# Kernel tuning notes

Hardware: AMD Instinct MI355X
Metric: run time of the kernel (lower is better)

## Reference

```python
import jax, jax.numpy as jnp
import numpy as np

B, N, H = 2, 4096, 1024
HEADS, DHEAD, M = 16, 64, 256
KERNEL_EPS = 1e-3


def setup_inputs() -> dict:
    key = jax.random.key(0)
    ks = jax.random.split(key, 10)
    w = lambda k, shp: jax.random.normal(k, shp, dtype=jnp.float32) * 0.02
    return {
        "hidden_states": jax.random.normal(ks[0], (B, N, H), dtype=jnp.float32),
        "Wq": w(ks[1], (H, H)), "bq": jnp.zeros((H,), jnp.float32),
        "Wk": w(ks[2], (H, H)), "bk": jnp.zeros((H,), jnp.float32),
        "Wv": w(ks[3], (H, H)), "bv": jnp.zeros((H,), jnp.float32),
        "Wo": w(ks[4], (H, H)), "bo": jnp.zeros((H,), jnp.float32),
        "proj": jax.random.normal(ks[5], (M, DHEAD), dtype=jnp.float32),
    }


def _split_heads(x):
    b, n, _ = x.shape
    return x.reshape(b, n, HEADS, DHEAD).transpose(0, 2, 1, 3)  # [b,h,n,d]


def _softmax_kernel(data, proj, is_query):
    # data: [b,h,n,d]; proj: [m,d]
    data_normalizer = DHEAD ** (-0.25)
    data_dash = jnp.einsum('bhnd,md->bhnm', data_normalizer * data, proj)
    diag_data = -0.5 * jnp.sum(data * data, axis=-1, keepdims=True)  # [b,h,n,1]
    if is_query:
        # argmax over a size-1 last dim -> stabilizer == diag_data itself
        stab = diag_data
    else:
        stab = jnp.max(diag_data)
    kernel_out = jnp.exp(diag_data + (data_dash - stab))  # exp kernel: exp(h + x)
    return (M ** (-0.5)) * (kernel_out + KERNEL_EPS)


def _performer_forward(hidden_states, Wq, bq, Wk, bk, Wv, bv, Wo, bo, proj):
    q = _split_heads(jnp.einsum('bni,oi->bno', hidden_states, Wq) + bq)
    k = _split_heads(jnp.einsum('bni,oi->bno', hidden_states, Wk) + bk)
    v = _split_heads(jnp.einsum('bni,oi->bno', hidden_states, Wv) + bv)

    qf = _softmax_kernel(q, proj, is_query=True)   # [b,h,n,m]
    kf = _softmax_kernel(k, proj, is_query=False)  # [b,h,n,m]

    # linear_attention (non-causal FAVOR+)
    k_cumsum = kf.sum(axis=-2)                                   # [b,h,m]
    d_inv = 1.0 / jnp.einsum('bhnm,bhm->bhn', qf, k_cumsum)      # [b,h,n]
    context = jnp.einsum('bhnm,bhne->bhme', kf, v)               # [b,h,m,d]
    out = jnp.einsum('bhme,bhnm,bhn->bhne', context, qf, d_inv)  # [b,h,n,d]

    out = out.transpose(0, 2, 1, 3).reshape(hidden_states.shape[0], -1, H)
    return jnp.einsum('bni,oi->bno', out, Wo) + bo


def reference(hidden_states, Wq, bq, Wk, bk, Wv, bv, Wo, bo, proj):
    return _performer_forward(hidden_states, Wq, bq, Wk, bk, Wv, bv, Wo, bo, proj)
```

## Files before the change

kernel.cpp:

```cpp
#include <hip/hip_runtime.h>
#include <math.h>

#define B_      2
#define N_      4096
#define H_      1024
#define HEADS_  16
#define DH_     64
#define M_      256
#define NSPLIT  8
#define EPAD    80

constexpr float NORMALIZER = 0.35355339059327373f;
constexpr float RATIO      = 0.0625f;
constexpr float KEPS       = 1e-3f;

typedef __bf16 bf16x8 __attribute__((ext_vector_type(8)));
typedef __bf16 bf16x4 __attribute__((ext_vector_type(4)));
typedef float  f32x4  __attribute__((ext_vector_type(4)));

__global__ __launch_bounds__(256) void split_bf16(
    const float* __restrict__ src, __bf16* __restrict__ hi, __bf16* __restrict__ lo)
{
    int i = blockIdx.x * 256 + threadIdx.x;
    float4 v = ((const float4*)src)[i];
    float vv[4] = {v.x, v.y, v.z, v.w};
    bf16x4 h, l;
#pragma unroll
    for (int j = 0; j < 4; ++j) {
        __bf16 hh = (__bf16)vv[j];
        h[j] = hh;
        l[j] = (__bf16)(vv[j] - (float)hh);
    }
    ((bf16x4*)hi)[i] = h;
    ((bf16x4*)lo)[i] = l;
}

__global__ __launch_bounds__(256) void split_w(
    const float* __restrict__ W0, const float* __restrict__ W1,
    const float* __restrict__ W2, const float* __restrict__ W3,
    __bf16* __restrict__ hi, __bf16* __restrict__ lo)
{
    const float* src = W0;
    if (blockIdx.y == 1) src = W1;
    else if (blockIdx.y == 2) src = W2;
    else if (blockIdx.y == 3) src = W3;
    int i = blockIdx.x * 256 + threadIdx.x;
    size_t o = (size_t)blockIdx.y * 262144 + i;
    float4 v = ((const float4*)src)[i];
    float vv[4] = {v.x, v.y, v.z, v.w};
    bf16x4 h, l;
#pragma unroll
    for (int j = 0; j < 4; ++j) {
        __bf16 hh = (__bf16)vv[j];
        h[j] = hh;
        l[j] = (__bf16)(vv[j] - (float)hh);
    }
    ((bf16x4*)hi)[o] = h;
    ((bf16x4*)lo)[o] = l;
}

__global__ __launch_bounds__(512, 2) void gemm_qkv(
    const __bf16* __restrict__ Ah, const __bf16* __restrict__ Al,
    const __bf16* __restrict__ WH, const __bf16* __restrict__ WL,
    const float* __restrict__ bq, const float* __restrict__ bk, const float* __restrict__ bv,
    __bf16* __restrict__ Qh, __bf16* __restrict__ Ql,
    __bf16* __restrict__ Kh, __bf16* __restrict__ Kl,
    __bf16* __restrict__ Vh, __bf16* __restrict__ Vl)
{
    __shared__ alignas(16) __bf16 lds[2][8][128 * 32];

    const int t    = threadIdx.x;
    const int lane = t & 63;
    const int lm   = lane & 15;
    const int lq   = lane >> 4;
    const int w    = t >> 6;
    const int wm   = (w >> 2) * 64;
    const int wn   = (w & 3) * 32;

    const int wg = blockIdx.x + 8 * blockIdx.y;
    const int sw = (wg & 7) * 64 + (wg >> 3);
    const int n0 = (sw & 7) * 128;
    const int m0 = (sw >> 3) * 128;
    const int K  = 1024;
    const int NK = 32;
    const size_t WSZ = (size_t)H_ * H_;

    const __bf16* mysrc;
    if      (w == 0) mysrc = Ah;
    else if (w == 1) mysrc = Al;
    else             mysrc = ((w & 1) ? WL : WH) + (size_t)((w - 2) >> 1) * WSZ;
    const int rbase  = (w < 2) ? m0 : n0;
    const int rsub   = lane >> 2;
    const int slot   = lane & 3;
    const int schunk = slot ^ ((lane >> 3) & 3);
    const __bf16* gbase = mysrc + (size_t)(rbase + rsub) * K + schunk * 8;

    f32x4 acc[3][4][2];
#pragma unroll
    for (int s = 0; s < 3; ++s)
#pragma unroll
        for (int i = 0; i < 4; ++i)
#pragma unroll
            for (int j = 0; j < 2; ++j) acc[s][i][j] = (f32x4){0.f, 0.f, 0.f, 0.f};

    const int swz = (lq ^ ((lm >> 1) & 3)) * 8;

    auto stage = [&](int buf, int k0) {
#pragma unroll
        for (int c = 0; c < 8; ++c) {
            const __bf16* g = gbase + (size_t)c * 16 * K + k0;
            __builtin_amdgcn_global_load_lds(
                (const __attribute__((address_space(1))) void*)g,
                (__attribute__((address_space(3))) void*)&lds[buf][w][c * 512],
                16, 0, 0);
        }
    };

    auto compute = [&](int p) {
        bf16x8 bh[3][2], bl[3][2];
#pragma unroll
        for (int s = 0; s < 3; ++s)
#pragma unroll
            for (int j = 0; j < 2; ++j) {
                int off = (wn + j * 16 + lm) * 32 + swz;
                bh[s][j] = *(const bf16x8*)&lds[p][2 + 2 * s][off];
                bl[s][j] = *(const bf16x8*)&lds[p][3 + 2 * s][off];
            }
#pragma unroll
        for (int i = 0; i < 4; ++i) {
            int off = (wm + i * 16 + lm) * 32 + swz;
            bf16x8 ah = *(const bf16x8*)&lds[p][0][off];
            bf16x8 al = *(const bf16x8*)&lds[p][1][off];
#pragma unroll
            for (int s = 0; s < 3; ++s)
#pragma unroll
                for (int j = 0; j < 2; ++j) {
                    acc[s][i][j] = __builtin_amdgcn_mfma_f32_16x16x32_bf16(ah, bh[s][j], acc[s][i][j], 0, 0, 0);
                    acc[s][i][j] = __builtin_amdgcn_mfma_f32_16x16x32_bf16(al, bh[s][j], acc[s][i][j], 0, 0, 0);
                    acc[s][i][j] = __builtin_amdgcn_mfma_f32_16x16x32_bf16(ah, bl[s][j], acc[s][i][j], 0, 0, 0);
                }
        }
    };

    stage(0, 0);
    int p = 0;
#pragma unroll 1
    for (int kk = 0; kk < NK - 1; ++kk) {
        stage(p ^ 1, (kk + 1) * 32);
        asm volatile("s_waitcnt vmcnt(8)" ::: "memory");
        asm volatile("s_barrier" ::: "memory");
        compute(p);
        asm volatile("s_barrier" ::: "memory");
        p ^= 1;
    }
    asm volatile("s_waitcnt vmcnt(0)" ::: "memory");
    asm volatile("s_barrier" ::: "memory");
    compute(p);

    const float* biases[3] = {bq, bk, bv};
    __bf16* Chs[3] = {Qh, Kh, Vh};
    __bf16* Cls[3] = {Ql, Kl, Vl};
#pragma unroll
    for (int s = 0; s < 3; ++s) {
        float bsr[2];
#pragma unroll
        for (int j = 0; j < 2; ++j) bsr[j] = biases[s][n0 + wn + j * 16 + lm];
#pragma unroll
        for (int i = 0; i < 4; ++i)
#pragma unroll
            for (int r = 0; r < 4; ++r) {
                int rowm = m0 + wm + i * 16 + lq * 4 + r;
#pragma unroll
                for (int j = 0; j < 2; ++j) {
                    int col = n0 + wn + j * 16 + lm;
                    float o = acc[s][i][j][r] + bsr[j];
                    __bf16 hh = (__bf16)o;
                    Chs[s][(size_t)rowm * 1024 + col] = hh;
                    Cls[s][(size_t)rowm * 1024 + col] = (__bf16)(o - (float)hh);
                }
            }
    }
}

__global__ __launch_bounds__(512, 4) void gemm_out(
    const __bf16* __restrict__ Ah, const __bf16* __restrict__ Al,
    const __bf16* __restrict__ Bh, const __bf16* __restrict__ Bl,
    const float* __restrict__ bias, float* __restrict__ C0)
{
    __shared__ alignas(16) __bf16 lds[2][4][128 * 32];

    const int t    = threadIdx.x;
    const int lane = t & 63;
    const int lm   = lane & 15;
    const int lq   = lane >> 4;
    const int w    = t >> 6;
    const int wm   = (w >> 2) * 64;
    const int wn   = (w & 3) * 32;

    const int wg = blockIdx.x + 8 * blockIdx.y;
    const int sw = (wg & 7) * 64 + (wg >> 3);
    const int n0 = (sw & 7) * 128;
    const int m0 = (sw >> 3) * 128;
    const int K  = 1024;
    const int NK = 32;

    const int tw = w >> 1;
    const int hw = w & 1;
    const __bf16* mysrc = (tw == 0) ? Ah : (tw == 1) ? Al : (tw == 2) ? Bh : Bl;
    const int     rbase = ((tw < 2) ? m0 : n0) + hw * 64;
    const int rsub   = lane >> 2;
    const int slot   = lane & 3;
    const int schunk = slot ^ ((lane >> 3) & 3);
    const __bf16* gbase = mysrc + (size_t)(rbase + rsub) * K + schunk * 8;

    f32x4 acc[4][2];
#pragma unroll
    for (int i = 0; i < 4; ++i)
#pragma unroll
        for (int j = 0; j < 2; ++j) acc[i][j] = (f32x4){0.f, 0.f, 0.f, 0.f};

    const int swz = (lq ^ ((lm >> 1) & 3)) * 8;

    auto stage = [&](int buf, int k0) {
#pragma unroll
        for (int c = 0; c < 4; ++c) {
            const __bf16* g = gbase + (size_t)c * 16 * K + k0;
            __builtin_amdgcn_global_load_lds(
                (const __attribute__((address_space(1))) void*)g,
                (__attribute__((address_space(3))) void*)&lds[buf][tw][(hw * 64 + c * 16) * 32],
                16, 0, 0);
        }
    };

    auto compute = [&](int p) {
        const __bf16* tAh = lds[p][0];
        const __bf16* tAl = lds[p][1];
        const __bf16* tBh = lds[p][2];
        const __bf16* tBl = lds[p][3];
        bf16x8 bh[2], bl[2];
#pragma unroll
        for (int j = 0; j < 2; ++j) {
            int off = (wn + j * 16 + lm) * 32 + swz;
            bh[j] = *(const bf16x8*)&tBh[off];
            bl[j] = *(const bf16x8*)&tBl[off];
        }
#pragma unroll
        for (int i = 0; i < 4; ++i) {
            int off = (wm + i * 16 + lm) * 32 + swz;
            bf16x8 ah = *(const bf16x8*)&tAh[off];
            bf16x8 al = *(const bf16x8*)&tAl[off];
#pragma unroll
            for (int j = 0; j < 2; ++j) {
                acc[i][j] = __builtin_amdgcn_mfma_f32_16x16x32_bf16(ah, bh[j], acc[i][j], 0, 0, 0);
                acc[i][j] = __builtin_amdgcn_mfma_f32_16x16x32_bf16(al, bh[j], acc[i][j], 0, 0, 0);
                acc[i][j] = __builtin_amdgcn_mfma_f32_16x16x32_bf16(ah, bl[j], acc[i][j], 0, 0, 0);
            }
        }
    };

    stage(0, 0);
    int p = 0;
#pragma unroll 1
    for (int kk = 0; kk < NK - 1; ++kk) {
        stage(p ^ 1, (kk + 1) * 32);
        asm volatile("s_waitcnt vmcnt(4)" ::: "memory");
        asm volatile("s_barrier" ::: "memory");
        compute(p);
        asm volatile("s_barrier" ::: "memory");
        p ^= 1;
    }
    asm volatile("s_waitcnt vmcnt(0)" ::: "memory");
    asm volatile("s_barrier" ::: "memory");
    compute(p);

    float bsr[2];
#pragma unroll
    for (int j = 0; j < 2; ++j) bsr[j] = bias[n0 + wn + j * 16 + lm];
#pragma unroll
    for (int i = 0; i < 4; ++i)
#pragma unroll
        for (int r = 0; r < 4; ++r) {
            int rowm = m0 + wm + i * 16 + lq * 4 + r;
#pragma unroll
            for (int j = 0; j < 2; ++j) {
                int col = n0 + wn + j * 16 + lm;
                C0[(size_t)rowm * 1024 + col] = acc[i][j][r] + bsr[j];
            }
        }
}

__global__ __launch_bounds__(256) void diag_kernel(
    const __bf16* __restrict__ Kh, const __bf16* __restrict__ Kl,
    float* __restrict__ diag, float* __restrict__ partials)
{
    int gt = blockIdx.x * 256 + threadIdx.x;
    int r  = gt >> 2;
    int q  = gt & 3;
    const bf16x8* ph = (const bf16x8*)(Kh + (size_t)r * 64 + q * 16);
    const bf16x8* pl = (const bf16x8*)(Kl + (size_t)r * 64 + q * 16);
    float s = 0.f;
#pragma unroll
    for (int i = 0; i < 2; ++i) {
        bf16x8 vh = ph[i], vl = pl[i];
#pragma unroll
        for (int j = 0; j < 8; ++j) {
            float x = (float)vh[j] + (float)vl[j];
            s += x * x;
        }
    }
    s += __shfl_xor(s, 1);
    s += __shfl_xor(s, 2);
    float d = -0.5f * s;
    if (q == 0) {
        int h = r & 15, bn = r >> 4;
        int n = bn & 4095, b = bn >> 12;
        diag[(((size_t)b * 16 + h) << 12) + n] = d;
    }
    __shared__ float red[256];
    red[threadIdx.x] = d;
    __syncthreads();
    for (int s2 = 128; s2 > 0; s2 >>= 1) {
        if (threadIdx.x < s2) red[threadIdx.x] = fmaxf(red[threadIdx.x], red[threadIdx.x + s2]);
        __syncthreads();
    }
    if (threadIdx.x == 0) partials[blockIdx.x] = red[0];
}

__global__ __launch_bounds__(256) void reduce_stab(
    const float* __restrict__ partials, float* __restrict__ stab, int n)
{
    float m = -3.0e38f;
    for (int i = threadIdx.x; i < n; i += 256) m = fmaxf(m, partials[i]);
    __shared__ float red[256];
    red[threadIdx.x] = m;
    __syncthreads();
    for (int s2 = 128; s2 > 0; s2 >>= 1) {
        if (threadIdx.x < s2) red[threadIdx.x] = fmaxf(red[threadIdx.x], red[threadIdx.x + s2]);
        __syncthreads();
    }
    if (threadIdx.x == 0) stab[0] = red[0];
}

__global__ __launch_bounds__(256, 2) void ctx_mfma(
    const __bf16* __restrict__ Kh, const __bf16* __restrict__ Kl,
    const __bf16* __restrict__ Vh, const __bf16* __restrict__ Vl,
    const __bf16* __restrict__ projH, const __bf16* __restrict__ projL,
    const float* __restrict__ diag, const float* __restrict__ stabp,
    float* __restrict__ ctxp)
{
    __shared__ alignas(16) char ldsbuf[59904];
    __shared__ float dg[64];
    __bf16* kfTh = (__bf16*)ldsbuf;
    __bf16* kfTl = kfTh + 9216;
    __bf16* vTh  = kfTl + 9216;
    __bf16* vTl  = vTh + 5760;
    float*  ctxe = (float*)ldsbuf;

    const int t    = threadIdx.x;
    const int lane = t & 63;
    const int w    = t >> 6;
    const int lm   = lane & 15;
    const int lq   = lane >> 4;
    const int bh   = blockIdx.z;
    const int b    = bh >> 4, h = bh & 15;
    const int mh   = blockIdx.y;
    const int slice = blockIdx.x;
    const int mwave = mh * 128 + w * 32;
    const float stab = stabp[0];
    const size_t rowbase = (size_t)b * N_ * H_ + (size_t)h * DH_;
    const float* diag_bh = diag + (size_t)bh * N_;

    for (int idx = t; idx < 16 * 72; idx += 256) {
        int e = 64 + idx / 72, n = idx % 72;
        vTh[e * 72 + n] = (e == 64 && n < 64) ? (__bf16)1.0f : (__bf16)0.0f;
        vTl[e * 72 + n] = (__bf16)0.0f;
    }

    bf16x8 ph[2][2], pl[2][2];
#pragma unroll
    for (int mf = 0; mf < 2; ++mf)
#pragma unroll
        for (int ks = 0; ks < 2; ++ks) {
            size_t pa = (size_t)(mwave + mf * 16 + lm) * 64 + ks * 32 + lq * 8;
            ph[mf][ks] = *(const bf16x8*)(projH + pa);
            pl[mf][ks] = *(const bf16x8*)(projL + pa);
        }

    f32x4 acc[2][5];
#pragma unroll
    for (int mf = 0; mf < 2; ++mf)
#pragma unroll
        for (int ef = 0; ef < 5; ++ef) acc[mf][ef] = (f32x4){0.f, 0.f, 0.f, 0.f};

    const int nl = t >> 2, dc = (t & 3) * 16;
    bf16x8 v0, v1, u0, u1;
    bf16x8 kh_p[4][2], kl_p[4][2];
    float dgr = 0.f;
    {
        const int nbase = slice * (N_ / NSPLIT);
        size_t va = rowbase + (size_t)(nbase + nl) * H_ + dc;
        v0 = *(const bf16x8*)(Vh + va);
        v1 = *(const bf16x8*)(Vh + va + 8);
        u0 = *(const bf16x8*)(Vl + va);
        u1 = *(const bf16x8*)(Vl + va + 8);
#pragma unroll
        for (int nf = 0; nf < 4; ++nf)
#pragma unroll
            for (int ks = 0; ks < 2; ++ks) {
                size_t ka = rowbase + (size_t)(nbase + nf * 16 + lm) * H_ + ks * 32 + lq * 8;
                kh_p[nf][ks] = *(const bf16x8*)(Kh + ka);
                kl_p[nf][ks] = *(const bf16x8*)(Kl + ka);
            }
        if (t < 64) dgr = diag_bh[nbase + t];
    }

    for (int tile = 0; tile < 8; ++tile) {
        const int n0 = slice * (N_ / NSPLIT) + tile * 64;
        __syncthreads();

#pragma unroll
        for (int j = 0; j < 8; ++j) {
            vTh[(dc + j) * 72 + nl]     = v0[j];
            vTh[(dc + 8 + j) * 72 + nl] = v1[j];
            vTl[(dc + j) * 72 + nl]     = u0[j];
            vTl[(dc + 8 + j) * 72 + nl] = u1[j];
        }
        if (t < 64) dg[t] = dgr - stab;

        f32x4 dsh[4][2];
#pragma unroll
        for (int nf = 0; nf < 4; ++nf) {
#pragma unroll
            for (int mf = 0; mf < 2; ++mf) dsh[nf][mf] = (f32x4){0.f, 0.f, 0.f, 0.f};
#pragma unroll
            for (int mf = 0; mf < 2; ++mf)
#pragma unroll
                for (int ks = 0; ks < 2; ++ks) {
                    dsh[nf][mf] = __builtin_amdgcn_mfma_f32_16x16x32_bf16(kh_p[nf][ks], ph[mf][ks], dsh[nf][mf], 0, 0, 0);
                    dsh[nf][mf] = __builtin_amdgcn_mfma_f32_16x16x32_bf16(kl_p[nf][ks], ph[mf][ks], dsh[nf][mf], 0, 0, 0);
                    dsh[nf][mf] = __builtin_amdgcn_mfma_f32_16x16x32_bf16(kh_p[nf][ks], pl[mf][ks], dsh[nf][mf], 0, 0, 0);
                }
        }

        __syncthreads();

        if (tile < 7) {
            size_t va = rowbase + (size_t)(n0 + 64 + nl) * H_ + dc;
            v0 = *(const bf16x8*)(Vh + va);
            v1 = *(const bf16x8*)(Vh + va + 8);
            u0 = *(const bf16x8*)(Vl + va);
            u1 = *(const bf16x8*)(Vl + va + 8);
#pragma unroll
            for (int nf = 0; nf < 4; ++nf)
#pragma unroll
                for (int ks = 0; ks < 2; ++ks) {
                    size_t ka = rowbase + (size_t)(n0 + 64 + nf * 16 + lm) * H_ + ks * 32 + lq * 8;
                    kh_p[nf][ks] = *(const bf16x8*)(Kh + ka);
                    kl_p[nf][ks] = *(const bf16x8*)(Kl + ka);
                }
            if (t < 64) dgr = diag_bh[n0 + 64 + t];
        }

#pragma unroll
        for (int nf = 0; nf < 4; ++nf) {
            float4 dgv = *(const float4*)&dg[nf * 16 + lq * 4];
            float dga[4] = {dgv.x, dgv.y, dgv.z, dgv.w};
#pragma unroll
            for (int mf = 0; mf < 2; ++mf) {
                int mrow = w * 32 + mf * 16 + lm;
                bf16x4 vh_, vl_;
#pragma unroll
                for (int r = 0; r < 4; ++r) {
                    float kf = RATIO * (__expf(dga[r] + NORMALIZER * dsh[nf][mf][r]) + KEPS);
                    __bf16 hh = (__bf16)kf;
                    vh_[r] = hh;
                    vl_[r] = (__bf16)(kf - (float)hh);
                }
                int nbase = nf * 16 + lq * 4;
                *(bf16x4*)&kfTh[mrow * 72 + nbase] = vh_;
                *(bf16x4*)&kfTl[mrow * 72 + nbase] = vl_;
            }
        }

#pragma unroll
        for (int ks = 0; ks < 2; ++ks) {
#pragma unroll
            for (int mf = 0; mf < 2; ++mf) {
                bf16x8 af = *(const bf16x8*)&kfTh[(w * 32 + mf * 16 + lm) * 72 + ks * 32 + lq * 8];
                bf16x8 afl = *(const bf16x8*)&kfTl[(w * 32 + mf * 16 + lm) * 72 + ks * 32 + lq * 8];
#pragma unroll
                for (int ef = 0; ef < 5; ++ef) {
                    bf16x8 bfh = *(const bf16x8*)&vTh[(ef * 16 + lm) * 72 + ks * 32 + lq * 8];
                    bf16x8 bfl = *(const bf16x8*)&vTl[(ef * 16 + lm) * 72 + ks * 32 + lq * 8];
                    acc[mf][ef] = __builtin_amdgcn_mfma_f32_16x16x32_bf16(af,  bfh, acc[mf][ef], 0, 0, 0);
                    acc[mf][ef] = __builtin_amdgcn_mfma_f32_16x16x32_bf16(afl, bfh, acc[mf][ef], 0, 0, 0);
                    acc[mf][ef] = __builtin_amdgcn_mfma_f32_16x16x32_bf16(af,  bfl, acc[mf][ef], 0, 0, 0);
                }
            }
        }
    }

    __syncthreads();
#pragma unroll
    for (int mf = 0; mf < 2; ++mf)
#pragma unroll
        for (int ef = 0; ef < 5; ++ef)
#pragma unroll
            for (int r = 0; r < 4; ++r) {
                int ml = w * 32 + mf * 16 + lq * 4 + r;
                int e  = ef * 16 + lm;
                ctxe[ml * 81 + e] = acc[mf][ef][r];
            }
    __syncthreads();
    const size_t SLICE = (size_t)(B_ * HEADS_) * EPAD * M_;
    const size_t obase = (size_t)slice * SLICE + (size_t)bh * EPAD * M_;
    for (int i = t; i < EPAD * 128; i += 256) {
        int e = i >> 7, ml = i & 127;
        ctxp[obase + (size_t)e * M_ + mh * 128 + ml] = ctxe[ml * 81 + e];
    }
}

__global__ __launch_bounds__(256) void ctx_reduce(
    const float* __restrict__ ctxp, __bf16* __restrict__ ctxTh, __bf16* __restrict__ ctxTl)
{
    int idx = blockIdx.x * 256 + threadIdx.x;
    const size_t SLICE = (size_t)(B_ * HEADS_) * EPAD * M_;
    float s = 0.f;
#pragma unroll
    for (int k = 0; k < NSPLIT; ++k) s += ctxp[(size_t)k * SLICE + idx];
    __bf16 hh = (__bf16)s;
    ctxTh[idx] = hh;
    ctxTl[idx] = (__bf16)(s - (float)hh);
}

__global__ __launch_bounds__(512, 2) void out_mfma(
    const __bf16* __restrict__ Qh, const __bf16* __restrict__ Ql,
    const __bf16* __restrict__ projH, const __bf16* __restrict__ projL,
    const __bf16* __restrict__ ctxTh, const __bf16* __restrict__ ctxTl,
    __bf16* __restrict__ attnH, __bf16* __restrict__ attnL)
{
    __shared__ alignas(16) __bf16 ctxLh[80 * 256];
    __shared__ alignas(16) __bf16 ctxLl[80 * 256];
    __shared__ alignas(16) __bf16 qfh[8][32][72];
    __shared__ alignas(16) __bf16 qfl[8][32][72];

    const int t    = threadIdx.x;
    const int lane = t & 63;
    const int w    = t >> 6;
    const int lm   = lane & 15;
    const int lq   = lane >> 4;
    const int bh   = blockIdx.y;
    const int b    = bh >> 4, h = bh & 15;
    const int nw   = blockIdx.x * 256 + w * 32;
    const size_t rowbase = (size_t)b * N_ * H_ + (size_t)h * DH_;

    const __bf16* cth = ctxTh + (size_t)bh * EPAD * M_;
    const __bf16* ctl = ctxTl + (size_t)bh * EPAD * M_;

    {
        const int r_in = lane >> 5;
        const int cp   = lane & 31;
#pragma unroll
        for (int c = 0; c < 5; ++c) {
            int idx = w * 5 + c;
            int r   = idx * 2 + r_in;
            int gc  = cp ^ (r & 7);
            const __bf16* gh = cth + (size_t)r * 256 + gc * 8;
            const __bf16* gl = ctl + (size_t)r * 256 + gc * 8;
            __builtin_amdgcn_global_load_lds(
                (const __attribute__((address_space(1))) void*)gh,
                (__attribute__((address_space(3))) void*)&ctxLh[idx * 512],
                16, 0, 0);
            __builtin_amdgcn_global_load_lds(
                (const __attribute__((address_space(1))) void*)gl,
                (__attribute__((address_space(3))) void*)&ctxLl[idx * 512],
                16, 0, 0);
        }
    }

    bf16x8 qh_[2][2], ql_[2][2];
#pragma unroll
    for (int nf = 0; nf < 2; ++nf)
#pragma unroll
        for (int ks = 0; ks < 2; ++ks) {
            size_t qa = rowbase + (size_t)(nw + nf * 16 + lm) * H_ + ks * 32 + lq * 8;
            qh_[nf][ks] = *(const bf16x8*)(Qh + qa);
            ql_[nf][ks] = *(const bf16x8*)(Ql + qa);
        }
    bf16x8 pc_h[4][2], pc_l[4][2];
#pragma unroll
    for (int mf = 0; mf < 4; ++mf)
#pragma unroll
        for (int ks = 0; ks < 2; ++ks) {
            size_t pa = (size_t)(mf * 16 + lm) * 64 + ks * 32 + lq * 8;
            pc_h[mf][ks] = *(const bf16x8*)(projH + pa);
            pc_l[mf][ks] = *(const bf16x8*)(projL + pa);
        }

    __syncthreads();

    f32x4 accO[2][5];
#pragma unroll
    for (int nf = 0; nf < 2; ++nf)
#pragma unroll
        for (int ef = 0; ef < 5; ++ef) accO[nf][ef] = (f32x4){0.f, 0.f, 0.f, 0.f};

#pragma unroll
    for (int mc = 0; mc < 4; ++mc) {
        const int m0 = mc * 64;
        f32x4 dsh[2][4];
#pragma unroll
        for (int nf = 0; nf < 2; ++nf)
#pragma unroll
            for (int mf = 0; mf < 4; ++mf) dsh[nf][mf] = (f32x4){0.f, 0.f, 0.f, 0.f};
#pragma unroll
        for (int mf = 0; mf < 4; ++mf)
#pragma unroll
            for (int ks = 0; ks < 2; ++ks)
#pragma unroll
                for (int nf = 0; nf < 2; ++nf) {
                    dsh[nf][mf] = __builtin_amdgcn_mfma_f32_16x16x32_bf16(qh_[nf][ks], pc_h[mf][ks], dsh[nf][mf], 0, 0, 0);
                    dsh[nf][mf] = __builtin_amdgcn_mfma_f32_16x16x32_bf16(ql_[nf][ks], pc_h[mf][ks], dsh[nf][mf], 0, 0, 0);
                    dsh[nf][mf] = __builtin_amdgcn_mfma_f32_16x16x32_bf16(qh_[nf][ks], pc_l[mf][ks], dsh[nf][mf], 0, 0, 0);
                }
        bf16x8 pn_h[4][2], pn_l[4][2];
        if (mc < 3) {
#pragma unroll
            for (int mf = 0; mf < 4; ++mf)
#pragma unroll
                for (int ks = 0; ks < 2; ++ks) {
                    size_t pa = (size_t)((m0 + 64) + mf * 16 + lm) * 64 + ks * 32 + lq * 8;
                    pn_h[mf][ks] = *(const bf16x8*)(projH + pa);
                    pn_l[mf][ks] = *(const bf16x8*)(projL + pa);
                }
        }
#pragma unroll
        for (int nf = 0; nf < 2; ++nf)
#pragma unroll
            for (int mf = 0; mf < 4; ++mf)
#pragma unroll
                for (int r = 0; r < 4; ++r) {
                    float qf = RATIO * (__expf(NORMALIZER * dsh[nf][mf][r]) + KEPS);
                    __bf16 hh = (__bf16)qf;
                    int nloc = nf * 16 + lq * 4 + r;
                    qfh[w][nloc][mf * 16 + lm] = hh;
                    qfl[w][nloc][mf * 16 + lm] = (__bf16)(qf - (float)hh);
                }
#pragma unroll
        for (int ks = 0; ks < 2; ++ks) {
            bf16x8 af[2], afl[2];
#pragma unroll
            for (int nf = 0; nf < 2; ++nf) {
                af[nf]  = *(const bf16x8*)&qfh[w][nf * 16 + lm][ks * 32 + lq * 8];
                afl[nf] = *(const bf16x8*)&qfl[w][nf * 16 + lm][ks * 32 + lq * 8];
            }
#pragma unroll
            for (int ef = 0; ef < 5; ++ef) {
                int row = ef * 16 + lm;
                int sc  = ((m0 >> 3) + ks * 4 + lq) ^ (lm & 7);
                int off = row * 256 + sc * 8;
                bf16x8 bfh = *(const bf16x8*)&ctxLh[off];
                bf16x8 bfl = *(const bf16x8*)&ctxLl[off];
#pragma unroll
                for (int nf = 0; nf < 2; ++nf) {
                    accO[nf][ef] = __builtin_amdgcn_mfma_f32_16x16x32_bf16(af[nf],  bfh, accO[nf][ef], 0, 0, 0);
                    accO[nf][ef] = __builtin_amdgcn_mfma_f32_16x16x32_bf16(afl[nf], bfh, accO[nf][ef], 0, 0, 0);
                    accO[nf][ef] = __builtin_amdgcn_mfma_f32_16x16x32_bf16(af[nf],  bfl, accO[nf][ef], 0, 0, 0);
                }
            }
        }
        if (mc < 3) {
#pragma unroll
            for (int mf = 0; mf < 4; ++mf)
#pragma unroll
                for (int ks = 0; ks < 2; ++ks) {
                    pc_h[mf][ks] = pn_h[mf][ks];
                    pc_l[mf][ks] = pn_l[mf][ks];
                }
        }
    }

#pragma unroll
    for (int nf = 0; nf < 2; ++nf) {
        float dinv[4];
#pragma unroll
        for (int r = 0; r < 4; ++r) {
            float den = __shfl(accO[nf][4][r], lane & 48);
            dinv[r] = 1.f / den;
        }
#pragma unroll
        for (int ef = 0; ef < 4; ++ef)
#pragma unroll
            for (int r = 0; r < 4; ++r) {
                float o = accO[nf][ef][r] * dinv[r];
                __bf16 hh = (__bf16)o;
                size_t oa = rowbase + (size_t)(nw + nf * 16 + lq * 4 + r) * H_ + ef * 16 + lm;
                attnH[oa] = hh;
                attnL[oa] = (__bf16)(o - (float)hh);
            }
    }
}

extern "C" void kernel_launch(void* const* d_in, const int* in_sizes, int n_in,
                              void* d_out, int out_size, void* d_ws, size_t ws_size,
                              hipStream_t stream) {
    const float* hs   = (const float*)d_in[0];
    const float* Wq   = (const float*)d_in[1];
    const float* bq   = (const float*)d_in[2];
    const float* Wk   = (const float*)d_in[3];
    const float* bk   = (const float*)d_in[4];
    const float* Wv   = (const float*)d_in[5];
    const float* bv   = (const float*)d_in[6];
    const float* Wo   = (const float*)d_in[7];
    const float* bo   = (const float*)d_in[8];
    const float* proj = (const float*)d_in[9];
    float* out = (float*)d_out;

    const size_t QSZ = (size_t)B_ * N_ * H_;
    const size_t WSZ = (size_t)H_ * H_;
    const size_t CTXT = (size_t)B_ * HEADS_ * EPAD * M_;

    __bf16* Qh  = (__bf16*)d_ws;
    __bf16* Ql  = Qh + QSZ;
    __bf16* Kh  = Ql + QSZ;
    __bf16* Kl  = Kh + QSZ;
    __bf16* Vh  = Kl + QSZ;
    __bf16* Vl  = Vh + QSZ;
    __bf16* hsH = Vl + QSZ;
    __bf16* hsL = hsH + QSZ;
    __bf16* WH  = hsL + QSZ;
    __bf16* WL  = WH + 4 * WSZ;
    __bf16* projH = WL + 4 * WSZ;
    __bf16* projL = projH + (size_t)M_ * DH_;
    __bf16* ctxTh = projL + (size_t)M_ * DH_;
    __bf16* ctxTl = ctxTh + CTXT;
    float*  diag  = (float*)(ctxTl + CTXT);
    float*  parts = diag + (size_t)B_ * HEADS_ * N_;
    float*  stab  = parts + 2048;
    float*  ctxp  = stab + 16;

    __bf16 *WoH = WH + 3*WSZ, *WoL = WL + 3*WSZ;

    split_bf16<<<QSZ / 4 / 256, 256, 0, stream>>>(hs, hsH, hsL);
    split_w<<<dim3(WSZ / 4 / 256, 4), 256, 0, stream>>>(Wq, Wk, Wv, Wo, WH, WL);
    split_bf16<<<(M_ * DH_) / 4 / 256, 256, 0, stream>>>(proj, projH, projL);

    gemm_qkv<<<dim3(H_ / 128, (B_ * N_) / 128), 512, 0, stream>>>(
        hsH, hsL, WH, WL, bq, bk, bv, Qh, Ql, Kh, Kl, Vh, Vl);

    diag_kernel<<<2048, 256, 0, stream>>>(Kh, Kl, diag, parts);
    reduce_stab<<<1, 256, 0, stream>>>(parts, stab, 2048);

    ctx_mfma<<<dim3(NSPLIT, 2, B_ * HEADS_), 256, 0, stream>>>(
        Kh, Kl, Vh, Vl, projH, projL, diag, stab, ctxp);

    ctx_reduce<<<(B_ * HEADS_ * EPAD * M_) / 256, 256, 0, stream>>>(ctxp, ctxTh, ctxTl);

    out_mfma<<<dim3(N_ / 256, B_ * HEADS_), 512, 0, stream>>>(
        Qh, Ql, projH, projL, ctxTh, ctxTl, hsH, hsL);

    gemm_out<<<dim3(H_ / 128, (B_ * N_) / 128), 512, 0, stream>>>(
        hsH, hsL, WoH, WoL, bo, out);
}
```

Before: 414.1 us.

## Split QKV GEMM k-step into three phased stages with staggered loads and priorities

The QKV projection main loop now runs each k-tile in three phases, one per output matrix (Q, K, V). Warps issue their next-tile global-to-LDS loads only after reading the current operands, and wait on them in the phase where that data is first needed. The goal is to spread load issue and waits across the MFMA work, cut register pressure by keeping only one output's B fragments live, and raise wave priority during MFMA bursts. In exchange there are three barriers per k-step instead of two, and the ordering between stage writes and other warps' LDS reads becomes delicate.

```diff
diff --git a/kernel.cpp b/kernel.cpp
--- a/kernel.cpp
+++ b/kernel.cpp
@@ -116,46 +116,79 @@
         }
     };
 
-    auto compute = [&](int p) {
-        bf16x8 bh[3][2], bl[3][2];
-#pragma unroll
-        for (int s = 0; s < 3; ++s)
-#pragma unroll
-            for (int j = 0; j < 2; ++j) {
-                int off = (wn + j * 16 + lm) * 32 + swz;
-                bh[s][j] = *(const bf16x8*)&lds[p][2 + 2 * s][off];
-                bl[s][j] = *(const bf16x8*)&lds[p][3 + 2 * s][off];
-            }
-#pragma unroll
-        for (int i = 0; i < 4; ++i) {
-            int off = (wm + i * 16 + lm) * 32 + swz;
-            bf16x8 ah = *(const bf16x8*)&lds[p][0][off];
-            bf16x8 al = *(const bf16x8*)&lds[p][1][off];
-#pragma unroll
-            for (int s = 0; s < 3; ++s)
-#pragma unroll
-                for (int j = 0; j < 2; ++j) {
-                    acc[s][i][j] = __builtin_amdgcn_mfma_f32_16x16x32_bf16(ah, bh[s][j], acc[s][i][j], 0, 0, 0);
-                    acc[s][i][j] = __builtin_amdgcn_mfma_f32_16x16x32_bf16(al, bh[s][j], acc[s][i][j], 0, 0, 0);
-                    acc[s][i][j] = __builtin_amdgcn_mfma_f32_16x16x32_bf16(ah, bl[s][j], acc[s][i][j], 0, 0, 0);
-                }
-        }
-    };
+#define MFMA_S(S) \
+    _Pragma("unroll") \
+    for (int i = 0; i < 4; ++i) \
+        _Pragma("unroll") \
+        for (int j = 0; j < 2; ++j) { \
+            acc[S][i][j] = __builtin_amdgcn_mfma_f32_16x16x32_bf16(ah[i], bh[j], acc[S][i][j], 0, 0, 0); \
+            acc[S][i][j] = __builtin_amdgcn_mfma_f32_16x16x32_bf16(al[i], bh[j], acc[S][i][j], 0, 0, 0); \
+            acc[S][i][j] = __builtin_amdgcn_mfma_f32_16x16x32_bf16(ah[i], bl[j], acc[S][i][j], 0, 0, 0); \
+        }
 
     stage(0, 0);
     int p = 0;
 #pragma unroll 1
-    for (int kk = 0; kk < NK - 1; ++kk) {
-        stage(p ^ 1, (kk + 1) * 32);
-        asm volatile("s_waitcnt vmcnt(8)" ::: "memory");
+    for (int kt = 0; kt < NK; ++kt) {
+        const int nb  = p ^ 1;
+        const int nk0 = (kt + 1) * 32;
+        const bool more = (kt < NK - 1);
+        bf16x8 ah[4], al[4], bh[2], bl[2];
+
+        if (w < 4) asm volatile("s_waitcnt vmcnt(0)" ::: "memory");
         asm volatile("s_barrier" ::: "memory");
-        compute(p);
+#pragma unroll
+        for (int i = 0; i < 4; ++i) {
+            int off = (wm + i * 16 + lm) * 32 + swz;
+            ah[i] = *(const bf16x8*)&lds[p][0][off];
+            al[i] = *(const bf16x8*)&lds[p][1][off];
+        }
+#pragma unroll
+        for (int j = 0; j < 2; ++j) {
+            int off = (wn + j * 16 + lm) * 32 + swz;
+            bh[j] = *(const bf16x8*)&lds[p][2][off];
+            bl[j] = *(const bf16x8*)&lds[p][3][off];
+        }
+        if (more && w < 4) stage(nb, nk0);
+        asm volatile("s_waitcnt lgkmcnt(0)" ::: "memory");
+        __builtin_amdgcn_sched_barrier(0);
+        __builtin_amdgcn_s_setprio(1);
+        MFMA_S(0)
+        __builtin_amdgcn_s_setprio(0);
+
+        if (w == 4 || w == 5) asm volatile("s_waitcnt vmcnt(0)" ::: "memory");
         asm volatile("s_barrier" ::: "memory");
+#pragma unroll
+        for (int j = 0; j < 2; ++j) {
+            int off = (wn + j * 16 + lm) * 32 + swz;
+            bh[j] = *(const bf16x8*)&lds[p][4][off];
+            bl[j] = *(const bf16x8*)&lds[p][5][off];
+        }
+        if (more && (w == 4 || w == 5)) stage(nb, nk0);
+        asm volatile("s_waitcnt lgkmcnt(0)" ::: "memory");
+        __builtin_amdgcn_sched_barrier(0);
+        __builtin_amdgcn_s_setprio(1);
+        MFMA_S(1)
+        __builtin_amdgcn_s_setprio(0);
+
+        if (w >= 6) asm volatile("s_waitcnt vmcnt(0)" ::: "memory");
+        asm volatile("s_barrier" ::: "memory");
+#pragma unroll
+        for (int j = 0; j < 2; ++j) {
+            int off = (wn + j * 16 + lm) * 32 + swz;
+            bh[j] = *(const bf16x8*)&lds[p][6][off];
+            bl[j] = *(const bf16x8*)&lds[p][7][off];
+        }
+        if (more && w >= 6) stage(nb, nk0);
+        asm volatile("s_waitcnt lgkmcnt(0)" ::: "memory");
+        __builtin_amdgcn_sched_barrier(0);
+        __builtin_amdgcn_s_setprio(1);
+        MFMA_S(2)
+        __builtin_amdgcn_s_setprio(0);
+
         p ^= 1;
     }
-    asm volatile("s_waitcnt vmcnt(0)" ::: "memory");
-    asm volatile("s_barrier" ::: "memory");
-    compute(p);
+#undef MFMA_S
 
     const float* biases[3] = {bq, bk, bv};
     __bf16* Chs[3] = {Qh, Kh, Vh};
```

Result: no change. 415.6 us (median of 2 runs) (+0.4%).
